# Optimization experiments

Hardware: AMD Instinct MI355X
Metric: run time of the kernel (lower is better)

The kernel has to match this reference:

```python
import jax, jax.numpy as jnp
import numpy as np

B, N, C, H = 8, 1024, 768, 12
D = C // H  # head_dim = 64
SCALE = D ** -0.5
EPS = 1e-5  # nn.LayerNorm default


def layer_norm(x, gamma, beta):
    # normalize over last dim (head_dim)
    mu = jnp.mean(x, axis=-1, keepdims=True)
    var = jnp.var(x, axis=-1, keepdims=True)
    return (x - mu) * jax.lax.rsqrt(var + EPS) * gamma + beta


def setup_inputs() -> dict:
    key = jax.random.key(0)
    ks = jax.random.split(key, 5)
    s = 0.02
    return {
        "x": jax.random.normal(ks[0], (B, N, C), jnp.float32),
        "qkv_w": jax.random.normal(ks[1], (3 * C, C), jnp.float32) * s,
        "qkv_b": jax.random.normal(ks[2], (3 * C,), jnp.float32) * s,
        "q_gamma": jnp.ones((D,), jnp.float32),
        "q_beta": jnp.zeros((D,), jnp.float32),
        "k_gamma": jnp.ones((D,), jnp.float32),
        "k_beta": jnp.zeros((D,), jnp.float32),
        "proj_w": jax.random.normal(ks[3], (C, C), jnp.float32) * s,
        "proj_b": jax.random.normal(ks[4], (C,), jnp.float32) * s,
    }


def reference(x, qkv_w, qkv_b, q_gamma, q_beta, k_gamma, k_beta, proj_w, proj_b):
    Bx, Nx, Cx = x.shape
    qkv = x @ qkv_w.T + qkv_b                       # [B,N,3C]
    qkv = qkv.reshape(Bx, Nx, 3, H, D).transpose(2, 0, 3, 1, 4)  # [3,B,H,N,D]
    q, k, v = qkv[0], qkv[1], qkv[2]
    q = layer_norm(q, q_gamma, q_beta) * SCALE
    k = layer_norm(k, k_gamma, k_beta)
    attn = jax.nn.softmax(jnp.einsum('bhnd,bhmd->bhnm', q, k), axis=-1)  # [B,H,N,N]
    # attn_drop is identity (p=0, eval)
    out = jnp.einsum('bhnm,bhmd->bhnd', attn, v)    # [B,H,N,D]
    out = out.transpose(0, 2, 1, 3).reshape(Bx, Nx, Cx)
    out = out @ proj_w.T + proj_b                   # proj_drop identity
    return out, attn
```

## Files before the change

kernel.cpp:

```cpp
#include <hip/hip_runtime.h>
#include <hip/hip_bf16.h>
#include <stdint.h>

typedef __bf16 bf16_t;
typedef __bf16 bf16x8 __attribute__((ext_vector_type(8)));
typedef __bf16 bf16x4 __attribute__((ext_vector_type(4)));
typedef float f32x4 __attribute__((ext_vector_type(4)));

#define DEV static __device__ __forceinline__

DEV f32x4 mfma16(bf16x8 a, bf16x8 b, f32x4 c) {
  return __builtin_amdgcn_mfma_f32_16x16x32_bf16(a, b, c, 0, 0, 0);
}

DEV void gll16(const void* g, void* l) {
  __builtin_amdgcn_global_load_lds(
      (const __attribute__((address_space(1))) uint32_t*)g,
      (__attribute__((address_space(3))) uint32_t*)l, 16, 0, 0);
}

DEV int swz128(int row, int c16) {
  return (row << 7) + (((c16 ^ row) & 7) << 4);
}
DEV int swzel128(int row, int col) {
  return (row << 7) + ((((col >> 3) ^ row) & 7) << 4) + ((col & 7) << 1);
}

__global__ void __launch_bounds__(256)
cast_all(const float* __restrict__ x, bf16_t* __restrict__ ox,
         const float* __restrict__ w1, bf16_t* __restrict__ ow1,
         const float* __restrict__ w2, bf16_t* __restrict__ ow2) {
  long i = (long)(blockIdx.x * 256 + threadIdx.x) * 8;
  const float* s; bf16_t* d; long off;
  if (i < 6291456L)      { s = x;  d = ox;  off = i; }
  else if (i < 8060928L) { s = w1; d = ow1; off = i - 6291456L; }
  else if (i < 8650752L) { s = w2; d = ow2; off = i - 8060928L; }
  else return;
  float4 a = *(const float4*)(s + off);
  float4 b = *(const float4*)(s + off + 4);
  bf16x8 v;
  v[0] = (bf16_t)a.x; v[1] = (bf16_t)a.y; v[2] = (bf16_t)a.z; v[3] = (bf16_t)a.w;
  v[4] = (bf16_t)b.x; v[5] = (bf16_t)b.y; v[6] = (bf16_t)b.z; v[7] = (bf16_t)b.w;
  *(bf16x8*)(d + off) = v;
}

#define C1Q 0.1803368801111244f

__global__ void __launch_bounds__(256, 2)
gemm_qkv_ln(const bf16_t* __restrict__ A, const bf16_t* __restrict__ Bw,
            const float* __restrict__ bias,
            const float* __restrict__ qg, const float* __restrict__ qb,
            const float* __restrict__ kg, const float* __restrict__ kb,
            bf16_t* __restrict__ qkv, int M, int N, int K) {
  __shared__ __align__(16) char As[8192];
  __shared__ __align__(16) char Bs[8192];
  const int tid = threadIdx.x;
  const int lane = tid & 63;
  const int wave = tid >> 6;
  const int wr = wave >> 1, wc = wave & 1;
  const int tileM = blockIdx.y << 7;
  const int tileN = blockIdx.x << 7;
  const int lrow = lane & 15, lk = lane >> 4;

  f32x4 acc[4][4];
  f32x4 z = {0.f, 0.f, 0.f, 0.f};
#pragma unroll
  for (int m = 0; m < 4; m++)
#pragma unroll
    for (int n = 0; n < 4; n++) acc[m][n] = z;

  const int srow = wave * 16 + (lane >> 2);
  const int sb = lane & 3;
  const bf16_t* Asrc0 = A + (long)(tileM + srow) * K + sb * 8;
  const bf16_t* Asrc1 = A + (long)(tileM + 64 + srow) * K + sb * 8;
  const bf16_t* Bsrc0 = Bw + (long)(tileN + srow) * K + sb * 8;
  const bf16_t* Bsrc1 = Bw + (long)(tileN + 64 + srow) * K + sb * 8;
  char* Adst = As + wave * 1024;
  char* Bdst = Bs + wave * 1024;

  for (int k0 = 0; k0 < K; k0 += 32) {
    __syncthreads();
    gll16(Asrc0 + k0, Adst);
    gll16(Asrc1 + k0, Adst + 4096);
    gll16(Bsrc0 + k0, Bdst);
    gll16(Bsrc1 + k0, Bdst + 4096);
    __syncthreads();
    bf16x8 af[4], bfr[4];
#pragma unroll
    for (int m = 0; m < 4; m++)
      af[m] = *(const bf16x8*)(As + (wr * 64 + m * 16 + lrow) * 64 + lk * 16);
#pragma unroll
    for (int n = 0; n < 4; n++)
      bfr[n] = *(const bf16x8*)(Bs + (wc * 64 + n * 16 + lrow) * 64 + lk * 16);
#pragma unroll
    for (int m = 0; m < 4; m++)
#pragma unroll
      for (int n = 0; n < 4; n++)
        acc[m][n] = mfma16(af[m], bfr[n], acc[m][n]);
  }

  const int t = tileN / 768;
  const int cbase = tileN + wc * 64;
  float g[4], be[4], bv[4];
#pragma unroll
  for (int n = 0; n < 4; n++) bv[n] = bias[cbase + n * 16 + lrow];
  if (t == 0) {
#pragma unroll
    for (int n = 0; n < 4; n++) {
      int d = n * 16 + lrow;
      g[n] = qg[d] * C1Q; be[n] = qb[d] * C1Q;
    }
  } else if (t == 1) {
#pragma unroll
    for (int n = 0; n < 4; n++) {
      int d = n * 16 + lrow;
      g[n] = kg[d]; be[n] = kb[d];
    }
  }

#pragma unroll
  for (int m = 0; m < 4; m++) {
#pragma unroll
    for (int r = 0; r < 4; r++) {
      float v[4];
#pragma unroll
      for (int n = 0; n < 4; n++) v[n] = acc[m][n][r] + bv[n];
      long row = tileM + wr * 64 + m * 16 + lk * 4 + r;
      bf16_t* dst = qkv + row * 2304 + cbase;
      if (t < 2) {
        float s = v[0] + v[1] + v[2] + v[3];
        float s2 = v[0]*v[0] + v[1]*v[1] + v[2]*v[2] + v[3]*v[3];
#pragma unroll
        for (int ofs = 1; ofs <= 8; ofs <<= 1) {
          s  += __shfl_xor(s, ofs);
          s2 += __shfl_xor(s2, ofs);
        }
        float mu = s * (1.f / 64.f);
        float rstd = rsqrtf(s2 * (1.f / 64.f) - mu * mu + 1e-5f);
#pragma unroll
        for (int n = 0; n < 4; n++)
          dst[n * 16 + lrow] = (bf16_t)((v[n] - mu) * rstd * g[n] + be[n]);
      } else {
#pragma unroll
        for (int n = 0; n < 4; n++)
          dst[n * 16 + lrow] = (bf16_t)v[n];
      }
    }
  }
}

__global__ void __launch_bounds__(256, 2)
gemm_bt(const bf16_t* __restrict__ A, const bf16_t* __restrict__ Bw,
        const float* __restrict__ bias, float* __restrict__ Cout,
        int M, int N, int K) {
  __shared__ __align__(16) char As[8192];
  __shared__ __align__(16) char Bs[8192];
  const int tid = threadIdx.x;
  const int lane = tid & 63;
  const int wave = tid >> 6;
  const int wr = wave >> 1, wc = wave & 1;
  const int tileM = blockIdx.y << 7;
  const int tileN = blockIdx.x << 7;
  const int lrow = lane & 15, lk = lane >> 4;

  f32x4 acc[4][4];
  f32x4 z = {0.f, 0.f, 0.f, 0.f};
#pragma unroll
  for (int m = 0; m < 4; m++)
#pragma unroll
    for (int n = 0; n < 4; n++) acc[m][n] = z;

  const int srow = wave * 16 + (lane >> 2);
  const int sb = lane & 3;
  const bf16_t* Asrc0 = A + (long)(tileM + srow) * K + sb * 8;
  const bf16_t* Asrc1 = A + (long)(tileM + 64 + srow) * K + sb * 8;
  const bf16_t* Bsrc0 = Bw + (long)(tileN + srow) * K + sb * 8;
  const bf16_t* Bsrc1 = Bw + (long)(tileN + 64 + srow) * K + sb * 8;
  char* Adst = As + wave * 1024;
  char* Bdst = Bs + wave * 1024;

  for (int k0 = 0; k0 < K; k0 += 32) {
    __syncthreads();
    gll16(Asrc0 + k0, Adst);
    gll16(Asrc1 + k0, Adst + 4096);
    gll16(Bsrc0 + k0, Bdst);
    gll16(Bsrc1 + k0, Bdst + 4096);
    __syncthreads();
    bf16x8 af[4], bfr[4];
#pragma unroll
    for (int m = 0; m < 4; m++)
      af[m] = *(const bf16x8*)(As + (wr * 64 + m * 16 + lrow) * 64 + lk * 16);
#pragma unroll
    for (int n = 0; n < 4; n++)
      bfr[n] = *(const bf16x8*)(Bs + (wc * 64 + n * 16 + lrow) * 64 + lk * 16);
#pragma unroll
    for (int m = 0; m < 4; m++)
#pragma unroll
      for (int n = 0; n < 4; n++)
        acc[m][n] = mfma16(af[m], bfr[n], acc[m][n]);
  }

  const int rg = lk;
#pragma unroll
  for (int n = 0; n < 4; n++) {
    int col = tileN + wc * 64 + n * 16 + lrow;
    float bv = bias[col];
#pragma unroll
    for (int m = 0; m < 4; m++) {
      long row0 = tileM + wr * 64 + m * 16 + rg * 4;
#pragma unroll
      for (int r = 0; r < 4; r++)
        Cout[(row0 + r) * N + col] = acc[m][n][r] + bv;
    }
  }
}

__global__ void __launch_bounds__(256, 2)
attn_kernel(const bf16_t* __restrict__ qkv, float* __restrict__ attn_out,
            bf16_t* __restrict__ out_heads) {
  const int tid = threadIdx.x;
  const int lane = tid & 63;
  const int wave = tid >> 6;
  const int lb = blockIdx.x;
  const int sid = (lb & 7) * 192 + (lb >> 3);
  const int qt = sid & 15;
  const int bh = sid >> 4;
  const int b = bh / 12, h = bh - b * 12;

  const bf16_t* base = qkv + (long)b * 2359296L + h * 64;
  const bf16_t* Qg = base;
  const bf16_t* Kg = base + 768;
  const bf16_t* Vg = base + 1536;

  __shared__ __align__(16) char Ks[8192];
  __shared__ __align__(16) char Vt[8192];
  __shared__ __align__(16) char QP[8192];

  const int lrow = lane & 15;
  const int lk = lane >> 4;
  const int sr = tid >> 2;
  const int sc = tid & 3;

  {
    const bf16_t* qp = Qg + (long)(qt * 64 + sr) * 2304 + sc * 8;
    const bf16_t* kp = Kg + (long)sr * 2304 + sc * 8;
    bf16x8 q0 = *(const bf16x8*)(qp);
    bf16x8 q1 = *(const bf16x8*)(qp + 32);
    bf16x8 k0 = *(const bf16x8*)(kp);
    bf16x8 k1 = *(const bf16x8*)(kp + 32);
    *(bf16x8*)(QP + swz128(sr, sc)) = q0;
    *(bf16x8*)(QP + swz128(sr, 4 + sc)) = q1;
    *(bf16x8*)(Ks + swz128(sr, sc)) = k0;
    *(bf16x8*)(Ks + swz128(sr, 4 + sc)) = k1;
  }
  __syncthreads();

  bf16x8 qf[2];
  qf[0] = *(const bf16x8*)(QP + swz128(wave * 16 + lrow, lk));
  qf[1] = *(const bf16x8*)(QP + swz128(wave * 16 + lrow, 4 + lk));

  auto computeS = [&](const char* Kb, f32x4 sfr[4]) {
    f32x4 z = {0.f, 0.f, 0.f, 0.f};
    sfr[0] = z; sfr[1] = z; sfr[2] = z; sfr[3] = z;
#pragma unroll
    for (int kk = 0; kk < 2; kk++)
#pragma unroll
      for (int f = 0; f < 4; f++) {
        bf16x8 kf = *(const bf16x8*)(Kb + swz128(f * 16 + lrow, kk * 4 + lk));
        sfr[f] = mfma16(qf[kk], kf, sfr[f]);
      }
  };

  float l_r[4] = {0.f, 0.f, 0.f, 0.f};

  for (int kt = 0; kt < 16; kt++) {
    const char* cur = (kt & 1) ? Vt : Ks;
    bf16x8 kr0, kr1;
    if (kt < 15) {
      const bf16_t* kp = Kg + (long)((kt + 1) * 64 + sr) * 2304 + sc * 8;
      kr0 = *(const bf16x8*)(kp);
      kr1 = *(const bf16x8*)(kp + 32);
    }
    f32x4 sfr[4];
    computeS(cur, sfr);
#pragma unroll
    for (int r = 0; r < 4; r++)
      l_r[r] += exp2f(sfr[0][r]) + exp2f(sfr[1][r]) +
                exp2f(sfr[2][r]) + exp2f(sfr[3][r]);
    if (kt < 15) {
      char* nxt = (kt & 1) ? Ks : Vt;
      *(bf16x8*)(nxt + swz128(sr, sc)) = kr0;
      *(bf16x8*)(nxt + swz128(sr, 4 + sc)) = kr1;
    }
    __syncthreads();
  }

  float il[4];
#pragma unroll
  for (int r = 0; r < 4; r++) {
#pragma unroll
    for (int ofs = 1; ofs <= 8; ofs <<= 1)
      l_r[r] += __shfl_xor(l_r[r], ofs);
    il[r] = 1.0f / l_r[r];
  }

  f32x4 of[4];
  {
    f32x4 z = {0.f, 0.f, 0.f, 0.f};
    of[0] = z; of[1] = z; of[2] = z; of[3] = z;
  }
  char* Pw = QP + wave * 2048;
  float* attn_base = attn_out + (long)bh * 1048576 + ((long)(qt * 64) << 10);

  const int vk = lane, vdg = wave;
  {
    const bf16_t* kp = Kg + (long)sr * 2304 + sc * 8;
    bf16x8 k0 = *(const bf16x8*)(kp);
    bf16x8 k1 = *(const bf16x8*)(kp + 32);
    const bf16_t* vp = Vg + (long)vk * 2304 + vdg * 16;
    bf16x8 v0 = *(const bf16x8*)(vp);
    bf16x8 v1 = *(const bf16x8*)(vp + 8);
    *(bf16x8*)(Ks + swz128(sr, sc)) = k0;
    *(bf16x8*)(Ks + swz128(sr, 4 + sc)) = k1;
#pragma unroll
    for (int j = 0; j < 8; j++) {
      *(bf16_t*)(Vt + swzel128(vdg * 16 + j, vk)) = v0[j];
      *(bf16_t*)(Vt + swzel128(vdg * 16 + 8 + j, vk)) = v1[j];
    }
  }
  __syncthreads();

  for (int kt = 0; kt < 16; kt++) {
    bf16x8 kr0, kr1, vr0, vr1;
    if (kt < 15) {
      const bf16_t* kp = Kg + (long)((kt + 1) * 64 + sr) * 2304 + sc * 8;
      kr0 = *(const bf16x8*)(kp);
      kr1 = *(const bf16x8*)(kp + 32);
      const bf16_t* vp = Vg + (long)((kt + 1) * 64 + vk) * 2304 + vdg * 16;
      vr0 = *(const bf16x8*)(vp);
      vr1 = *(const bf16x8*)(vp + 8);
    }
    f32x4 sfr[4];
    computeS(Ks, sfr);
#pragma unroll
    for (int f = 0; f < 4; f++)
#pragma unroll
      for (int r = 0; r < 4; r++) {
        float p = exp2f(sfr[f][r]) * il[r];
        *(bf16_t*)(Pw + swzel128(lk * 4 + r, f * 16 + lrow)) = (bf16_t)p;
      }
#pragma unroll
    for (int kk = 0; kk < 2; kk++) {
      bf16x8 pf = *(const bf16x8*)(Pw + swz128(lrow, kk * 4 + lk));
#pragma unroll
      for (int f = 0; f < 4; f++) {
        bf16x8 vf = *(const bf16x8*)(Vt + swz128(f * 16 + lrow, kk * 4 + lk));
        of[f] = mfma16(pf, vf, of[f]);
      }
    }
    float* ab = attn_base + kt * 64;
    {
      const int rsub = lane >> 4;
      const int c8 = lane & 15;
      const char* psrc = Pw + (c8 & 1) * 8;
#pragma unroll
      for (int i = 0; i < 4; i++) {
        int rl = i * 4 + rsub;
        bf16x4 pv = *(const bf16x4*)(psrc + swz128(rl, c8 >> 1));
        f32x4 v = {(float)pv[0], (float)pv[1], (float)pv[2], (float)pv[3]};
        __builtin_nontemporal_store(
            v, (f32x4*)(ab + ((long)(wave * 16 + rl) << 10) + c8 * 4));
      }
    }
    __syncthreads();
    if (kt < 15) {
      *(bf16x8*)(Ks + swz128(sr, sc)) = kr0;
      *(bf16x8*)(Ks + swz128(sr, 4 + sc)) = kr1;
#pragma unroll
      for (int j = 0; j < 8; j++) {
        *(bf16_t*)(Vt + swzel128(vdg * 16 + j, vk)) = vr0[j];
        *(bf16_t*)(Vt + swzel128(vdg * 16 + 8 + j, vk)) = vr1[j];
      }
    }
    __syncthreads();
  }

#pragma unroll
  for (int f = 0; f < 4; f++)
#pragma unroll
    for (int r = 0; r < 4; r++) {
      int nrow = qt * 64 + wave * 16 + lk * 4 + r;
      int d = f * 16 + lrow;
      out_heads[((long)b * 1024 + nrow) * 768 + h * 64 + d] = (bf16_t)of[f][r];
    }
}

extern "C" void kernel_launch(void* const* d_in, const int* in_sizes, int n_in,
                              void* d_out, int out_size, void* d_ws, size_t ws_size,
                              hipStream_t stream) {
  (void)in_sizes; (void)n_in; (void)out_size; (void)ws_size;
  const float* x       = (const float*)d_in[0];
  const float* qkv_w   = (const float*)d_in[1];
  const float* qkv_b   = (const float*)d_in[2];
  const float* q_gamma = (const float*)d_in[3];
  const float* q_beta  = (const float*)d_in[4];
  const float* k_gamma = (const float*)d_in[5];
  const float* k_beta  = (const float*)d_in[6];
  const float* proj_w  = (const float*)d_in[7];
  const float* proj_b  = (const float*)d_in[8];
  float* out = (float*)d_out;

  char* ws = (char*)d_ws;
  bf16_t* x_bf      = (bf16_t*)(ws);
  bf16_t* wqkv      = (bf16_t*)(ws + 12582912L);
  bf16_t* wproj     = (bf16_t*)(ws + 16121856L);
  bf16_t* qkv       = (bf16_t*)(ws + 17301504L);
  bf16_t* out_heads = (bf16_t*)(ws + 55050240L);

  cast_all<<<4224, 256, 0, stream>>>(x, x_bf, qkv_w, wqkv, proj_w, wproj);
  gemm_qkv_ln<<<dim3(18, 64), 256, 0, stream>>>(x_bf, wqkv, qkv_b,
                                                q_gamma, q_beta, k_gamma, k_beta,
                                                qkv, 8192, 2304, 768);
  attn_kernel<<<1536, 256, 0, stream>>>(qkv, out + 6291456L, out_heads);
  gemm_bt<<<dim3(6, 64), 256, 0, stream>>>(out_heads, wproj, proj_b, out, 8192, 768, 768);
}
```

Measured before the change: 189.0 us.

## Double attention query tile to 128 rows per block to reuse K/V tiles

Each attention block now handles 128 query rows instead of 64, with every wave computing two 16-row fragments that share the same K and V fragments loaded from LDS. This halves the number of blocks and halves the global K/V reloads across both passes, and reuses each K/V LDS fragment for two MFMAs. In exchange it increases register pressure (doubled accumulators) and LDS to 32KB per block, and leaves only 768 blocks, which may reduce occupancy and latency hiding.

```diff
diff --git a/kernel.cpp b/kernel.cpp
--- a/kernel.cpp
+++ b/kernel.cpp
@@ -222,9 +222,9 @@
   const int lane = tid & 63;
   const int wave = tid >> 6;
   const int lb = blockIdx.x;
-  const int sid = (lb & 7) * 192 + (lb >> 3);
-  const int qt = sid & 15;
-  const int bh = sid >> 4;
+  const int sid = (lb & 7) * 96 + (lb >> 3);
+  const int qt = sid & 7;
+  const int bh = sid >> 3;
   const int b = bh / 12, h = bh - b * 12;
 
   const bf16_t* base = qkv + (long)b * 2359296L + h * 64;
@@ -232,46 +232,61 @@
   const bf16_t* Kg = base + 768;
   const bf16_t* Vg = base + 1536;
 
+  __shared__ __align__(16) char QP[16384];
   __shared__ __align__(16) char Ks[8192];
   __shared__ __align__(16) char Vt[8192];
-  __shared__ __align__(16) char QP[8192];
 
   const int lrow = lane & 15;
   const int lk = lane >> 4;
+  const int w32 = wave * 32;
   const int sr = tid >> 2;
   const int sc = tid & 3;
 
   {
-    const bf16_t* qp = Qg + (long)(qt * 64 + sr) * 2304 + sc * 8;
+#pragma unroll
+    for (int q = 0; q < 2; q++) {
+      const bf16_t* qp = Qg + (long)(qt * 128 + q * 64 + sr) * 2304 + sc * 8;
+      bf16x8 q0 = *(const bf16x8*)(qp);
+      bf16x8 q1 = *(const bf16x8*)(qp + 32);
+      *(bf16x8*)(QP + swz128(q * 64 + sr, sc)) = q0;
+      *(bf16x8*)(QP + swz128(q * 64 + sr, 4 + sc)) = q1;
+    }
     const bf16_t* kp = Kg + (long)sr * 2304 + sc * 8;
-    bf16x8 q0 = *(const bf16x8*)(qp);
-    bf16x8 q1 = *(const bf16x8*)(qp + 32);
     bf16x8 k0 = *(const bf16x8*)(kp);
     bf16x8 k1 = *(const bf16x8*)(kp + 32);
-    *(bf16x8*)(QP + swz128(sr, sc)) = q0;
-    *(bf16x8*)(QP + swz128(sr, 4 + sc)) = q1;
     *(bf16x8*)(Ks + swz128(sr, sc)) = k0;
     *(bf16x8*)(Ks + swz128(sr, 4 + sc)) = k1;
   }
   __syncthreads();
 
-  bf16x8 qf[2];
-  qf[0] = *(const bf16x8*)(QP + swz128(wave * 16 + lrow, lk));
-  qf[1] = *(const bf16x8*)(QP + swz128(wave * 16 + lrow, 4 + lk));
-
-  auto computeS = [&](const char* Kb, f32x4 sfr[4]) {
+  bf16x8 qf[2][2];
+#pragma unroll
+  for (int rf = 0; rf < 2; rf++)
+#pragma unroll
+    for (int kk = 0; kk < 2; kk++)
+      qf[rf][kk] = *(const bf16x8*)(QP + swz128(w32 + rf * 16 + lrow, kk * 4 + lk));
+
+  auto computeS = [&](const char* Kb, f32x4 sfr[2][4]) {
     f32x4 z = {0.f, 0.f, 0.f, 0.f};
-    sfr[0] = z; sfr[1] = z; sfr[2] = z; sfr[3] = z;
-#pragma unroll
-    for (int kk = 0; kk < 2; kk++)
-#pragma unroll
-      for (int f = 0; f < 4; f++) {
-        bf16x8 kf = *(const bf16x8*)(Kb + swz128(f * 16 + lrow, kk * 4 + lk));
-        sfr[f] = mfma16(qf[kk], kf, sfr[f]);
-      }
+#pragma unroll
+    for (int rf = 0; rf < 2; rf++)
+#pragma unroll
+      for (int f = 0; f < 4; f++) sfr[rf][f] = z;
+#pragma unroll
+    for (int kk = 0; kk < 2; kk++) {
+      bf16x8 kf[4];
+#pragma unroll
+      for (int f = 0; f < 4; f++)
+        kf[f] = *(const bf16x8*)(Kb + swz128(f * 16 + lrow, kk * 4 + lk));
+#pragma unroll
+      for (int rf = 0; rf < 2; rf++)
+#pragma unroll
+        for (int f = 0; f < 4; f++)
+          sfr[rf][f] = mfma16(qf[rf][kk], kf[f], sfr[rf][f]);
+    }
   };
 
-  float l_r[4] = {0.f, 0.f, 0.f, 0.f};
+  float l_r[2][4] = {{0.f,0.f,0.f,0.f},{0.f,0.f,0.f,0.f}};
 
   for (int kt = 0; kt < 16; kt++) {
     const char* cur = (kt & 1) ? Vt : Ks;
@@ -281,12 +296,14 @@
       kr0 = *(const bf16x8*)(kp);
       kr1 = *(const bf16x8*)(kp + 32);
     }
-    f32x4 sfr[4];
+    f32x4 sfr[2][4];
     computeS(cur, sfr);
 #pragma unroll
-    for (int r = 0; r < 4; r++)
-      l_r[r] += exp2f(sfr[0][r]) + exp2f(sfr[1][r]) +
-                exp2f(sfr[2][r]) + exp2f(sfr[3][r]);
+    for (int rf = 0; rf < 2; rf++)
+#pragma unroll
+      for (int r = 0; r < 4; r++)
+        l_r[rf][r] += exp2f(sfr[rf][0][r]) + exp2f(sfr[rf][1][r]) +
+                      exp2f(sfr[rf][2][r]) + exp2f(sfr[rf][3][r]);
     if (kt < 15) {
       char* nxt = (kt & 1) ? Ks : Vt;
       *(bf16x8*)(nxt + swz128(sr, sc)) = kr0;
@@ -295,22 +312,27 @@
     __syncthreads();
   }
 
-  float il[4];
-#pragma unroll
-  for (int r = 0; r < 4; r++) {
-#pragma unroll
-    for (int ofs = 1; ofs <= 8; ofs <<= 1)
-      l_r[r] += __shfl_xor(l_r[r], ofs);
-    il[r] = 1.0f / l_r[r];
-  }
-
-  f32x4 of[4];
+  float il[2][4];
+#pragma unroll
+  for (int rf = 0; rf < 2; rf++)
+#pragma unroll
+    for (int r = 0; r < 4; r++) {
+      float l = l_r[rf][r];
+#pragma unroll
+      for (int ofs = 1; ofs <= 8; ofs <<= 1) l += __shfl_xor(l, ofs);
+      il[rf][r] = 1.0f / l;
+    }
+
+  f32x4 of[2][4];
   {
     f32x4 z = {0.f, 0.f, 0.f, 0.f};
-    of[0] = z; of[1] = z; of[2] = z; of[3] = z;
-  }
-  char* Pw = QP + wave * 2048;
-  float* attn_base = attn_out + (long)bh * 1048576 + ((long)(qt * 64) << 10);
+#pragma unroll
+    for (int rf = 0; rf < 2; rf++)
+#pragma unroll
+      for (int f = 0; f < 4; f++) of[rf][f] = z;
+  }
+  char* Pw = QP + wave * 4096;
+  float* attn_base = attn_out + (long)bh * 1048576 + ((long)(qt * 128) << 10);
 
   const int vk = lane, vdg = wave;
   {
@@ -340,22 +362,29 @@
       vr0 = *(const bf16x8*)(vp);
       vr1 = *(const bf16x8*)(vp + 8);
     }
-    f32x4 sfr[4];
+    f32x4 sfr[2][4];
     computeS(Ks, sfr);
 #pragma unroll
-    for (int f = 0; f < 4; f++)
-#pragma unroll
-      for (int r = 0; r < 4; r++) {
-        float p = exp2f(sfr[f][r]) * il[r];
-        *(bf16_t*)(Pw + swzel128(lk * 4 + r, f * 16 + lrow)) = (bf16_t)p;
-      }
+    for (int rf = 0; rf < 2; rf++)
+#pragma unroll
+      for (int f = 0; f < 4; f++)
+#pragma unroll
+        for (int r = 0; r < 4; r++) {
+          float p = exp2f(sfr[rf][f][r]) * il[rf][r];
+          *(bf16_t*)(Pw + swzel128(rf * 16 + lk * 4 + r, f * 16 + lrow)) = (bf16_t)p;
+        }
 #pragma unroll
     for (int kk = 0; kk < 2; kk++) {
-      bf16x8 pf = *(const bf16x8*)(Pw + swz128(lrow, kk * 4 + lk));
+      bf16x8 pf[2];
+#pragma unroll
+      for (int rf = 0; rf < 2; rf++)
+        pf[rf] = *(const bf16x8*)(Pw + swz128(rf * 16 + lrow, kk * 4 + lk));
 #pragma unroll
       for (int f = 0; f < 4; f++) {
         bf16x8 vf = *(const bf16x8*)(Vt + swz128(f * 16 + lrow, kk * 4 + lk));
-        of[f] = mfma16(pf, vf, of[f]);
+#pragma unroll
+        for (int rf = 0; rf < 2; rf++)
+          of[rf][f] = mfma16(pf[rf], vf, of[rf][f]);
       }
     }
     float* ab = attn_base + kt * 64;
@@ -364,12 +393,12 @@
       const int c8 = lane & 15;
       const char* psrc = Pw + (c8 & 1) * 8;
 #pragma unroll
-      for (int i = 0; i < 4; i++) {
+      for (int i = 0; i < 8; i++) {
         int rl = i * 4 + rsub;
         bf16x4 pv = *(const bf16x4*)(psrc + swz128(rl, c8 >> 1));
         f32x4 v = {(float)pv[0], (float)pv[1], (float)pv[2], (float)pv[3]};
         __builtin_nontemporal_store(
-            v, (f32x4*)(ab + ((long)(wave * 16 + rl) << 10) + c8 * 4));
+            v, (f32x4*)(ab + ((long)(w32 + rl) << 10) + c8 * 4));
       }
     }
     __syncthreads();
@@ -386,13 +415,15 @@
   }
 
 #pragma unroll
-  for (int f = 0; f < 4; f++)
-#pragma unroll
-    for (int r = 0; r < 4; r++) {
-      int nrow = qt * 64 + wave * 16 + lk * 4 + r;
-      int d = f * 16 + lrow;
-      out_heads[((long)b * 1024 + nrow) * 768 + h * 64 + d] = (bf16_t)of[f][r];
-    }
+  for (int rf = 0; rf < 2; rf++)
+#pragma unroll
+    for (int f = 0; f < 4; f++)
+#pragma unroll
+      for (int r = 0; r < 4; r++) {
+        int nrow = qt * 128 + w32 + rf * 16 + lk * 4 + r;
+        int d = f * 16 + lrow;
+        out_heads[((long)b * 1024 + nrow) * 768 + h * 64 + d] = (bf16_t)of[rf][f][r];
+      }
 }
 
 extern "C" void kernel_launch(void* const* d_in, const int* in_sizes, int n_in,
@@ -421,6 +452,6 @@
   gemm_qkv_ln<<<dim3(18, 64), 256, 0, stream>>>(x_bf, wqkv, qkv_b,
                                                 q_gamma, q_beta, k_gamma, k_beta,
                                                 qkv, 8192, 2304, 768);
-  attn_kernel<<<1536, 256, 0, stream>>>(qkv, out + 6291456L, out_heads);
+  attn_kernel<<<768, 256, 0, stream>>>(qkv, out + 6291456L, out_heads);
   gemm_bt<<<dim3(6, 64), 256, 0, stream>>>(out_heads, wproj, proj_b, out, 8192, 768, 768);
 }
```

After: 203.8 us. 7.8% more time.
